# Performance work log

Hardware: AMD Instinct MI355X
Metric: run time of the kernel (lower is better)

Reference implementation:

```python
import jax, jax.numpy as jnp
import numpy as np

H = 512   # hidden_size
IN = 5    # input_size
OUT = 2   # output_size
B = 2048
T_HIST = 50


def _lstm_cell(x, h, c, W_ih, W_hh, b_ih, b_hh):
    # PyTorch gate order: i, f, g, o
    z = x @ W_ih.T + h @ W_hh.T + (b_ih + b_hh)
    i, f, g, o = jnp.split(z, 4, axis=-1)
    i = jax.nn.sigmoid(i)
    f = jax.nn.sigmoid(f)
    g = jnp.tanh(g)
    o = jax.nn.sigmoid(o)
    c2 = f * c + i * g
    h2 = o * jnp.tanh(c2)
    return h2, c2


def setup_inputs() -> dict:
    key = jax.random.key(0)
    ks = jax.random.split(key, 20)
    s = 0.05
    inp = {
        "history": jax.random.normal(ks[0], (B, T_HIST, IN), dtype=jnp.float32),
        "future_frames": 30,
        # encoder layer 0 (input IN) and layer 1 (input H)
        "enc_W_ih0": jax.random.normal(ks[1], (4 * H, IN)) * s,
        "enc_W_hh0": jax.random.normal(ks[2], (4 * H, H)) * s,
        "enc_b_ih0": jnp.zeros((4 * H,), jnp.float32),
        "enc_b_hh0": jnp.zeros((4 * H,), jnp.float32),
        "enc_W_ih1": jax.random.normal(ks[3], (4 * H, H)) * s,
        "enc_W_hh1": jax.random.normal(ks[4], (4 * H, H)) * s,
        "enc_b_ih1": jnp.zeros((4 * H,), jnp.float32),
        "enc_b_hh1": jnp.zeros((4 * H,), jnp.float32),
        # decoder layer 0 (input OUT) and layer 1 (input H)
        "dec_W_ih0": jax.random.normal(ks[5], (4 * H, OUT)) * s,
        "dec_W_hh0": jax.random.normal(ks[6], (4 * H, H)) * s,
        "dec_b_ih0": jnp.zeros((4 * H,), jnp.float32),
        "dec_b_hh0": jnp.zeros((4 * H,), jnp.float32),
        "dec_W_ih1": jax.random.normal(ks[7], (4 * H, H)) * s,
        "dec_W_hh1": jax.random.normal(ks[8], (4 * H, H)) * s,
        "dec_b_ih1": jnp.zeros((4 * H,), jnp.float32),
        "dec_b_hh1": jnp.zeros((4 * H,), jnp.float32),
        # output head
        "out_W": jax.random.normal(ks[9], (OUT, H)) * s,
        "out_b": jnp.zeros((OUT,), jnp.float32),
    }
    return inp


def reference(history, enc_W_ih0, enc_W_hh0, enc_b_ih0, enc_b_hh0,
              enc_W_ih1, enc_W_hh1, enc_b_ih1, enc_b_hh1,
              dec_W_ih0, dec_W_hh0, dec_b_ih0, dec_b_hh0,
              dec_W_ih1, dec_W_hh1, dec_b_ih1, dec_b_hh1,
              out_W, out_b, future_frames):
    batch = history.shape[0]
    z = jnp.zeros((batch, H), history.dtype)

    # ----- encoder: 2-layer LSTM over history, scan over time -----
    def enc_step(carry, x_t):
        h0, c0, h1, c1 = carry
        h0, c0 = _lstm_cell(x_t, h0, c0, enc_W_ih0, enc_W_hh0, enc_b_ih0, enc_b_hh0)
        h1, c1 = _lstm_cell(h0, h1, c1, enc_W_ih1, enc_W_hh1, enc_b_ih1, enc_b_hh1)
        return (h0, c0, h1, c1), None

    xs = jnp.swapaxes(history, 0, 1)  # [T, B, IN]
    (h0, c0, h1, c1), _ = jax.lax.scan(enc_step, (z, z, z, z), xs)

    def dec_step(carry, _):
        h0, c0, h1, c1, x_prev = carry
        h0, c0 = _lstm_cell(x_prev, h0, c0, dec_W_ih0, dec_W_hh0, dec_b_ih0, dec_b_hh0)
        h1, c1 = _lstm_cell(h0, h1, c1, dec_W_ih1, dec_W_hh1, dec_b_ih1, dec_b_hh1)
        pred = h1 @ out_W.T + out_b  # [B, OUT]
        return (h0, c0, h1, c1, pred), pred

    x0 = jnp.zeros((batch, OUT), history.dtype)
    _, preds = jax.lax.scan(dec_step, (h0, c0, h1, c1, x0), None, length=future_frames)
    return jnp.swapaxes(preds, 0, 1)  # [B, T_fut, OUT]
```

## Files before the change

kernel.cpp:

```cpp
#include <hip/hip_runtime.h>
#include <hip/hip_bf16.h>


#define HDIM 512
#define BDIM 2048
#define T_HIST 50
#define T_FUT 30

typedef __attribute__((ext_vector_type(8))) short short8;
typedef __attribute__((ext_vector_type(4))) float f32x4;

#define AS1(p) ((const __attribute__((address_space(1))) void*)(p))
#define AS3(p) ((__attribute__((address_space(3))) void*)(p))

__device__ __forceinline__ ushort f2bf(float f) {
    union { float f; unsigned u; } v; v.f = f;
    unsigned r = v.u + 0x7fff + ((v.u >> 16) & 1);
    return (ushort)(r >> 16);
}
__device__ __forceinline__ float bf2f(ushort h) {
    union { unsigned u; float f; } v; v.u = ((unsigned)h) << 16;
    return v.f;
}

__device__ __forceinline__ int swz(int row, int slot) {
    int q = row >> 1;
    int t = ((row & 1) << 2) | slot;
    return q * 8 + (t ^ (q & 7));
}

struct SplitSrc { const float* src[6]; };

__global__ __launch_bounds__(256) void split_weights(SplitSrc s, ushort* __restrict__ hi,
                                                     ushort* __restrict__ lo) {
    int row = blockIdx.x;
    int j = blockIdx.y;
    int g = row >> 9, u = row & 511;
    int rp = (u >> 5) * 128 + ((u >> 4) & 1) * 64 + g * 16 + (u & 15);
    const float* S = s.src[j] + (size_t)row * HDIM;
    ushort* H = hi + ((size_t)j * 2048 + rp) * HDIM;
    ushort* L = lo + ((size_t)j * 2048 + rp) * HDIM;
    for (int k = threadIdx.x; k < HDIM; k += 256) {
        float w = S[k];
        ushort hb = f2bf(w);
        H[k] = hb;
        L[k] = f2bf(w - bf2f(hb));
    }
}

struct CellDesc {
    const ushort *A1h, *A1l, *W1h, *W1l;
    const ushort *A2h, *A2l, *W2h, *W2l;
    const float *x; const float *Wx;
    const float *bih, *bhh;
    float* c; ushort *hh; ushort *hl;
    int np, xs, Kx;
};

__global__ __launch_bounds__(256, 2) void lstm_cells(CellDesc dA, CellDesc dB) {
    __shared__ __align__(16) ushort lds[2 * 16384];

    const CellDesc d = (blockIdx.x >> 8) ? dB : dA;

    const int tid = threadIdx.x;
    const int w = tid >> 6, l = tid & 63;
    const int wm = w >> 1, wn = w & 1;
    const int lrow = l & 15, lk = l >> 4;

    int id = blockIdx.x & 255;
    int xcd = id & 7, rr = id >> 3;
    int bx = (xcd & 3) * 4 + (rr & 3);
    int by = (xcd >> 2) * 8 + (rr >> 2);
    const int m0 = by * 128;
    const int n0 = bx * 128;
    const int u  = bx * 32 + wn * 16 + lrow;

    f32x4 acc[4][4];

    #pragma unroll
    for (int g = 0; g < 4; ++g) {
        float b = d.bih[g * HDIM + u] + d.bhh[g * HDIM + u];
        f32x4 bv = {b, b, b, b};
        #pragma unroll
        for (int fm = 0; fm < 4; ++fm) acc[fm][g] = bv;
    }
    if (d.Kx > 0) {
        for (int kx = 0; kx < d.Kx; ++kx) {
            float wv[4];
            #pragma unroll
            for (int g = 0; g < 4; ++g) wv[g] = d.Wx[(size_t)(g * HDIM + u) * d.Kx + kx];
            #pragma unroll
            for (int fm = 0; fm < 4; ++fm)
                #pragma unroll
                for (int r = 0; r < 4; ++r) {
                    int m = m0 + wm * 64 + fm * 16 + lk * 4 + r;
                    float xv = d.x[(size_t)m * d.xs + kx];
                    #pragma unroll
                    for (int g = 0; g < 4; ++g) acc[fm][g][r] += xv * wv[g];
                }
        }
    }

    auto STAGE = [&](int t) {
        int buf = t & 1;
        int p = t >> 4;
        int kc = (t & 15) * 32;
        const ushort* Ah = p ? d.A2h : d.A1h;
        const ushort* Al = p ? d.A2l : d.A1l;
        const ushort* Bh = p ? d.W2h : d.W1h;
        const ushort* Bl = p ? d.W2l : d.W1l;
        ushort* base = &lds[buf * 16384];
        #pragma unroll
        for (int it = 0; it < 2; ++it) {
            int db = (w * 2 + it) * 64;
            int dd = db + l;
            int q = dd >> 3, tp = dd & 7;
            int tl = tp ^ (q & 7);
            int r = (q << 1) | (tl >> 2);
            int s = tl & 3;
            size_t go = (size_t)r * HDIM + kc + s * 8;
            __builtin_amdgcn_global_load_lds(AS1(Ah + (size_t)m0 * HDIM + go),
                                             AS3(base + db * 8), 16, 0, 0);
            __builtin_amdgcn_global_load_lds(AS1(Al + (size_t)m0 * HDIM + go),
                                             AS3(base + 4096 + db * 8), 16, 0, 0);
            __builtin_amdgcn_global_load_lds(AS1(Bh + (size_t)n0 * HDIM + go),
                                             AS3(base + 8192 + db * 8), 16, 0, 0);
            __builtin_amdgcn_global_load_lds(AS1(Bl + (size_t)n0 * HDIM + go),
                                             AS3(base + 12288 + db * 8), 16, 0, 0);
        }
    };

    const int nch = d.np * 16;
    STAGE(0);

    for (int t = 0; t < nch; ++t) {
        __syncthreads();
        if (t + 1 < nch) STAGE(t + 1);
        ushort* base = &lds[(t & 1) * 16384];
        short8 ah[4], al[4], bh[4], bl[4];
        #pragma unroll
        for (int fm = 0; fm < 4; ++fm) {
            int row = wm * 64 + fm * 16 + lrow;
            int off = swz(row, lk) * 8;
            ah[fm] = *(const short8*)(base + off);
            al[fm] = *(const short8*)(base + 4096 + off);
        }
        #pragma unroll
        for (int g = 0; g < 4; ++g) {
            int row = wn * 64 + g * 16 + lrow;
            int off = swz(row, lk) * 8;
            bh[g] = *(const short8*)(base + 8192 + off);
            bl[g] = *(const short8*)(base + 12288 + off);
        }
        #pragma unroll
        for (int fm = 0; fm < 4; ++fm)
            #pragma unroll
            for (int g = 0; g < 4; ++g)
                acc[fm][g] = __builtin_amdgcn_mfma_f32_16x16x32_bf16(
                    ah[fm], bh[g], acc[fm][g], 0, 0, 0);
        #pragma unroll
        for (int fm = 0; fm < 4; ++fm)
            #pragma unroll
            for (int g = 0; g < 4; ++g)
                acc[fm][g] = __builtin_amdgcn_mfma_f32_16x16x32_bf16(
                    al[fm], bh[g], acc[fm][g], 0, 0, 0);
        #pragma unroll
        for (int fm = 0; fm < 4; ++fm)
            #pragma unroll
            for (int g = 0; g < 4; ++g)
                acc[fm][g] = __builtin_amdgcn_mfma_f32_16x16x32_bf16(
                    ah[fm], bl[g], acc[fm][g], 0, 0, 0);
    }

    #pragma unroll
    for (int fm = 0; fm < 4; ++fm)
        #pragma unroll
        for (int r = 0; r < 4; ++r) {
            int m = m0 + wm * 64 + fm * 16 + lk * 4 + r;
            size_t idx = (size_t)m * HDIM + u;
            float zi = acc[fm][0][r], zf = acc[fm][1][r];
            float zg = acc[fm][2][r], zo = acc[fm][3][r];
            float ig = 1.f / (1.f + __expf(-zi));
            float fg = 1.f / (1.f + __expf(-zf));
            float gg = 2.f / (1.f + __expf(-2.f * zg)) - 1.f;
            float og = 1.f / (1.f + __expf(-zo));
            float cn = fg * d.c[idx] + ig * gg;
            float hn = og * (2.f / (1.f + __expf(-2.f * cn)) - 1.f);
            d.c[idx] = cn;
            ushort hb = f2bf(hn);
            d.hh[idx] = hb;
            d.hl[idx] = f2bf(hn - bf2f(hb));
        }
}

__global__ __launch_bounds__(256) void head_kernel(
    const ushort* __restrict__ hhi, const ushort* __restrict__ hlo,
    const float* __restrict__ Wout, const float* __restrict__ bout,
    float* __restrict__ out, float* __restrict__ xbuf, int t)
{
    int wave = (blockIdx.x * 256 + threadIdx.x) >> 6;
    int lane = threadIdx.x & 63;
    const ushort* hr = hhi + (size_t)wave * HDIM;
    const ushort* lr = hlo + (size_t)wave * HDIM;
    float s0 = 0.f, s1 = 0.f;
    #pragma unroll
    for (int k = lane; k < HDIM; k += 64) {
        float hv = bf2f(hr[k]) + bf2f(lr[k]);
        s0 += hv * Wout[k];
        s1 += hv * Wout[HDIM + k];
    }
    #pragma unroll
    for (int off = 32; off > 0; off >>= 1) {
        s0 += __shfl_down(s0, off);
        s1 += __shfl_down(s1, off);
    }
    if (lane == 0) {
        float p0 = s0 + bout[0], p1 = s1 + bout[1];
        out[(size_t)wave * (T_FUT * 2) + t * 2 + 0] = p0;
        out[(size_t)wave * (T_FUT * 2) + t * 2 + 1] = p1;
        xbuf[wave * 2 + 0] = p0;
        xbuf[wave * 2 + 1] = p1;
    }
}

extern "C" void kernel_launch(void* const* d_in, const int* in_sizes, int n_in,
                              void* d_out, int out_size, void* d_ws, size_t ws_size,
                              hipStream_t stream) {
    const float* history = (const float*)d_in[0];
    const float* eWih0 = (const float*)d_in[2];
    const float* eWhh0 = (const float*)d_in[3];
    const float* ebih0 = (const float*)d_in[4];
    const float* ebhh0 = (const float*)d_in[5];
    const float* eWih1 = (const float*)d_in[6];
    const float* eWhh1 = (const float*)d_in[7];
    const float* ebih1 = (const float*)d_in[8];
    const float* ebhh1 = (const float*)d_in[9];
    const float* dWih0 = (const float*)d_in[10];
    const float* dWhh0 = (const float*)d_in[11];
    const float* dbih0 = (const float*)d_in[12];
    const float* dbhh0 = (const float*)d_in[13];
    const float* dWih1 = (const float*)d_in[14];
    const float* dWhh1 = (const float*)d_in[15];
    const float* dbih1 = (const float*)d_in[16];
    const float* dbhh1 = (const float*)d_in[17];
    const float* outW  = (const float*)d_in[18];
    const float* outb  = (const float*)d_in[19];
    float* out = (float*)d_out;

    const size_t M = (size_t)2048 * 512;
    ushort* whi = (ushort*)d_ws;
    ushort* wlo = whi + 6 * M;
    ushort* hb  = wlo + 6 * M;
    float*  c0  = (float*)(hb + 8 * M);
    float*  c1  = c0 + M;
    float*  xbuf = c1 + M;

    ushort* h0a_hi = hb + 0 * M; ushort* h0a_lo = hb + 1 * M;
    ushort* h0b_hi = hb + 2 * M; ushort* h0b_lo = hb + 3 * M;
    ushort* h1a_hi = hb + 4 * M; ushort* h1a_lo = hb + 5 * M;
    ushort* h1b_hi = hb + 6 * M; ushort* h1b_lo = hb + 7 * M;

    hipMemsetAsync(h0a_hi, 0, 2 * M * sizeof(ushort), stream);
    hipMemsetAsync(h1a_hi, 0, 2 * M * sizeof(ushort), stream);
    hipMemsetAsync(c0, 0, 2 * M * sizeof(float), stream);
    hipMemsetAsync(xbuf, 0, BDIM * 2 * sizeof(float), stream);

    SplitSrc ss;
    ss.src[0] = eWhh0; ss.src[1] = eWih1; ss.src[2] = eWhh1;
    ss.src[3] = dWhh0; ss.src[4] = dWih1; ss.src[5] = dWhh1;
    split_weights<<<dim3(2048, 6), 256, 0, stream>>>(ss, whi, wlo);

    #define WHI(j) (whi + (size_t)(j) * M)
    #define WLO(j) (wlo + (size_t)(j) * M)

    auto H0R_HI = [&](int s){ return (s & 1) ? h0b_hi : h0a_hi; };
    auto H0R_LO = [&](int s){ return (s & 1) ? h0b_lo : h0a_lo; };
    auto H0W_HI = [&](int s){ return (s & 1) ? h0a_hi : h0b_hi; };
    auto H0W_LO = [&](int s){ return (s & 1) ? h0a_lo : h0b_lo; };
    auto H1R_HI = [&](int s){ return (s & 1) ? h1b_hi : h1a_hi; };
    auto H1R_LO = [&](int s){ return (s & 1) ? h1b_lo : h1a_lo; };
    auto H1W_HI = [&](int s){ return (s & 1) ? h1a_hi : h1b_hi; };
    auto H1W_LO = [&](int s){ return (s & 1) ? h1a_lo : h1b_lo; };

    auto mkL0enc = [&](int s) {
        CellDesc d{};
        d.A1h = H0R_HI(s); d.A1l = H0R_LO(s); d.W1h = WHI(0); d.W1l = WLO(0);
        d.np = 1; d.x = history + s * 5; d.xs = T_HIST * 5; d.Kx = 5; d.Wx = eWih0;
        d.bih = ebih0; d.bhh = ebhh0; d.c = c0; d.hh = H0W_HI(s); d.hl = H0W_LO(s);
        return d;
    };
    auto mkL1enc = [&](int s) {
        CellDesc d{};
        d.A1h = H0W_HI(s); d.A1l = H0W_LO(s); d.W1h = WHI(1); d.W1l = WLO(1);
        d.A2h = H1R_HI(s); d.A2l = H1R_LO(s); d.W2h = WHI(2); d.W2l = WLO(2);
        d.np = 2; d.Kx = 0; d.xs = 0;
        d.bih = ebih1; d.bhh = ebhh1; d.c = c1; d.hh = H1W_HI(s); d.hl = H1W_LO(s);
        return d;
    };
    auto mkD0 = [&](int s) {
        CellDesc d{};
        d.A1h = H0R_HI(s); d.A1l = H0R_LO(s); d.W1h = WHI(3); d.W1l = WLO(3);
        d.np = 1; d.x = xbuf; d.xs = 2; d.Kx = 2; d.Wx = dWih0;
        d.bih = dbih0; d.bhh = dbhh0; d.c = c0; d.hh = H0W_HI(s); d.hl = H0W_LO(s);
        return d;
    };
    auto mkD1 = [&](int s) {
        CellDesc d{};
        d.A1h = H0W_HI(s); d.A1l = H0W_LO(s); d.W1h = WHI(4); d.W1l = WLO(4);
        d.A2h = H1R_HI(s); d.A2l = H1R_LO(s); d.W2h = WHI(5); d.W2l = WLO(5);
        d.np = 2; d.Kx = 0; d.xs = 0;
        d.bih = dbih1; d.bhh = dbhh1; d.c = c1; d.hh = H1W_HI(s); d.hl = H1W_LO(s);
        return d;
    };

    dim3 blk(256);

    {
        CellDesc d = mkL0enc(0);
        lstm_cells<<<256, blk, 0, stream>>>(d, d);
    }
    for (int s = 0; s < T_HIST; ++s) {
        CellDesc dL1 = mkL1enc(s);
        CellDesc dNx = (s + 1 < T_HIST) ? mkL0enc(s + 1) : mkD0(T_HIST);
        lstm_cells<<<512, blk, 0, stream>>>(dL1, dNx);
    }
    for (int s = T_HIST; s < T_HIST + T_FUT; ++s) {
        CellDesc d1 = mkD1(s);
        lstm_cells<<<256, blk, 0, stream>>>(d1, d1);
        head_kernel<<<512, blk, 0, stream>>>(H1W_HI(s), H1W_LO(s), outW, outb,
                                             out, xbuf, s - T_HIST);
        if (s + 1 < T_HIST + T_FUT) {
            CellDesc d0 = mkD0(s + 1);
            lstm_cells<<<256, blk, 0, stream>>>(d0, d0);
        }
    }
    #undef WHI
    #undef WLO
}
```

Measured before the change: 3.772 ms.

## Fuse output head into decoder layer-0 cell and load weights directly to registers

The per-step head kernel launch is removed. Each decoder layer-0 cell block now recomputes the previous step's projection for its 128 rows, keeps it in LDS as the fed-back input, and the bx==0 blocks write it to the output. Only the final step still uses the standalone head kernel. The GEMM loop also stops staging weight tiles through LDS: it loads them straight from global memory into registers, double-buffered, which halves the LDS footprint and the LDS traffic. The cost is that the head dot products are recomputed redundantly across the 16 column blocks, and the register-loaded weight fragments raise register pressure.

```diff
diff --git a/kernel.cpp b/kernel.cpp
--- a/kernel.cpp
+++ b/kernel.cpp
@@ -53,12 +53,15 @@
     const ushort *A2h, *A2l, *W2h, *W2l;
     const float *x; const float *Wx;
     const float *bih, *bhh;
+    const ushort *hsrc_hi, *hsrc_lo;
+    const float *Wout, *bout; float *out_t;
     float* c; ushort *hh; ushort *hl;
     int np, xs, Kx;
 };
 
 __global__ __launch_bounds__(256, 2) void lstm_cells(CellDesc dA, CellDesc dB) {
-    __shared__ __align__(16) ushort lds[2 * 16384];
+    __shared__ __align__(16) ushort lds[2 * 8192];
+    __shared__ float xlds[128][2];
 
     const CellDesc d = (blockIdx.x >> 8) ? dB : dA;
 
@@ -75,7 +78,87 @@
     const int n0 = bx * 128;
     const int u  = bx * 32 + wn * 16 + lrow;
 
+    size_t boff[4];
+    #pragma unroll
+    for (int g = 0; g < 4; ++g)
+        boff[g] = (size_t)(n0 + wn * 64 + g * 16 + lrow) * HDIM + lk * 8;
+
     f32x4 acc[4][4];
+
+#define STAGE(t)                                                              \
+    {                                                                         \
+        int p_ = (t) >> 4;                                                    \
+        int kc_ = ((t) & 15) * 32;                                            \
+        const ushort* Ah_ = p_ ? d.A2h : d.A1h;                               \
+        const ushort* Al_ = p_ ? d.A2l : d.A1l;                               \
+        ushort* sb_ = &lds[((t) & 1) * 8192];                                 \
+        _Pragma("unroll")                                                     \
+        for (int it = 0; it < 2; ++it) {                                      \
+            int db = (w * 2 + it) * 64;                                       \
+            int dd = db + l;                                                  \
+            int q_ = dd >> 3, tp_ = dd & 7;                                   \
+            int tl_ = tp_ ^ (q_ & 7);                                         \
+            int r_ = (q_ << 1) | (tl_ >> 2);                                  \
+            int s_ = tl_ & 3;                                                 \
+            size_t go_ = (size_t)(m0 + r_) * HDIM + kc_ + s_ * 8;             \
+            __builtin_amdgcn_global_load_lds(AS1(Ah_ + go_),                  \
+                                             AS3(sb_ + db * 8), 16, 0, 0);    \
+            __builtin_amdgcn_global_load_lds(AS1(Al_ + go_),                  \
+                                             AS3(sb_ + 4096 + db * 8), 16, 0, 0); \
+        }                                                                     \
+    }
+
+#define LOADB(t, bh_, bl_)                                                    \
+    {                                                                         \
+        int p_ = (t) >> 4;                                                    \
+        int kc_ = ((t) & 15) * 32;                                            \
+        const ushort* Bh_ = p_ ? d.W2h : d.W1h;                               \
+        const ushort* Bl_ = p_ ? d.W2l : d.W1l;                               \
+        _Pragma("unroll")                                                     \
+        for (int g = 0; g < 4; ++g) {                                         \
+            bh_[g] = *(const short8*)(Bh_ + boff[g] + kc_);                   \
+            bl_[g] = *(const short8*)(Bl_ + boff[g] + kc_);                   \
+        }                                                                     \
+    }
+
+#define ITER(t, bhc, blc, bhn, bln)                                           \
+    {                                                                         \
+        __syncthreads();                                                      \
+        if ((t) + 1 < nch) { STAGE((t) + 1); LOADB((t) + 1, bhn, bln); }      \
+        ushort* base = &lds[((t) & 1) * 8192];                                \
+        short8 ah[4], al[4];                                                  \
+        _Pragma("unroll")                                                     \
+        for (int fm = 0; fm < 4; ++fm) {                                      \
+            int row_ = wm * 64 + fm * 16 + lrow;                              \
+            int off_ = swz(row_, lk) * 8;                                     \
+            ah[fm] = *(const short8*)(base + off_);                           \
+            al[fm] = *(const short8*)(base + 4096 + off_);                    \
+        }                                                                     \
+        _Pragma("unroll")                                                     \
+        for (int fm = 0; fm < 4; ++fm)                                        \
+            _Pragma("unroll")                                                 \
+            for (int g = 0; g < 4; ++g)                                       \
+                acc[fm][g] = __builtin_amdgcn_mfma_f32_16x16x32_bf16(         \
+                    ah[fm], bhc[g], acc[fm][g], 0, 0, 0);                     \
+        _Pragma("unroll")                                                     \
+        for (int fm = 0; fm < 4; ++fm)                                        \
+            _Pragma("unroll")                                                 \
+            for (int g = 0; g < 4; ++g)                                       \
+                acc[fm][g] = __builtin_amdgcn_mfma_f32_16x16x32_bf16(         \
+                    al[fm], bhc[g], acc[fm][g], 0, 0, 0);                     \
+        _Pragma("unroll")                                                     \
+        for (int fm = 0; fm < 4; ++fm)                                        \
+            _Pragma("unroll")                                                 \
+            for (int g = 0; g < 4; ++g)                                       \
+                acc[fm][g] = __builtin_amdgcn_mfma_f32_16x16x32_bf16(         \
+                    ah[fm], blc[g], acc[fm][g], 0, 0, 0);                     \
+    }
+
+    const int nch = d.np * 16;
+
+    short8 bh0[4], bl0[4], bh1[4], bl1[4];
+    STAGE(0);
+    LOADB(0, bh0, bl0);
 
     #pragma unroll
     for (int g = 0; g < 4; ++g) {
@@ -84,6 +167,7 @@
         #pragma unroll
         for (int fm = 0; fm < 4; ++fm) acc[fm][g] = bv;
     }
+
     if (d.Kx > 0) {
         for (int kx = 0; kx < d.Kx; ++kx) {
             float wv[4];
@@ -101,75 +185,51 @@
         }
     }
 
-    auto STAGE = [&](int t) {
-        int buf = t & 1;
-        int p = t >> 4;
-        int kc = (t & 15) * 32;
-        const ushort* Ah = p ? d.A2h : d.A1h;
-        const ushort* Al = p ? d.A2l : d.A1l;
-        const ushort* Bh = p ? d.W2h : d.W1h;
-        const ushort* Bl = p ? d.W2l : d.W1l;
-        ushort* base = &lds[buf * 16384];
-        #pragma unroll
-        for (int it = 0; it < 2; ++it) {
-            int db = (w * 2 + it) * 64;
-            int dd = db + l;
-            int q = dd >> 3, tp = dd & 7;
-            int tl = tp ^ (q & 7);
-            int r = (q << 1) | (tl >> 2);
-            int s = tl & 3;
-            size_t go = (size_t)r * HDIM + kc + s * 8;
-            __builtin_amdgcn_global_load_lds(AS1(Ah + (size_t)m0 * HDIM + go),
-                                             AS3(base + db * 8), 16, 0, 0);
-            __builtin_amdgcn_global_load_lds(AS1(Al + (size_t)m0 * HDIM + go),
-                                             AS3(base + 4096 + db * 8), 16, 0, 0);
-            __builtin_amdgcn_global_load_lds(AS1(Bh + (size_t)n0 * HDIM + go),
-                                             AS3(base + 8192 + db * 8), 16, 0, 0);
-            __builtin_amdgcn_global_load_lds(AS1(Bl + (size_t)n0 * HDIM + go),
-                                             AS3(base + 12288 + db * 8), 16, 0, 0);
-        }
-    };
-
-    const int nch = d.np * 16;
-    STAGE(0);
-
-    for (int t = 0; t < nch; ++t) {
+    if (d.hsrc_hi) {
+        int row = tid >> 1, half = tid & 1;
+        const ushort* hh = d.hsrc_hi + (size_t)(m0 + row) * HDIM + half * 256;
+        const ushort* hl = d.hsrc_lo + (size_t)(m0 + row) * HDIM + half * 256;
+        float s0 = 0.f, s1 = 0.f;
+        #pragma unroll 4
+        for (int j = 0; j < 32; ++j) {
+            short8 a = *(const short8*)(hh + j * 8);
+            short8 b = *(const short8*)(hl + j * 8);
+            #pragma unroll
+            for (int e = 0; e < 8; ++e) {
+                float hv = bf2f((ushort)a[e]) + bf2f((ushort)b[e]);
+                int k = half * 256 + j * 8 + e;
+                s0 += hv * d.Wout[k];
+                s1 += hv * d.Wout[HDIM + k];
+            }
+        }
+        s0 += __shfl_xor(s0, 1);
+        s1 += __shfl_xor(s1, 1);
+        float x0 = s0 + d.bout[0], x1 = s1 + d.bout[1];
+        if (half == 0) {
+            xlds[row][0] = x0; xlds[row][1] = x1;
+            if (bx == 0 && d.out_t) {
+                d.out_t[(size_t)(m0 + row) * (T_FUT * 2) + 0] = x0;
+                d.out_t[(size_t)(m0 + row) * (T_FUT * 2) + 1] = x1;
+            }
+        }
         __syncthreads();
-        if (t + 1 < nch) STAGE(t + 1);
-        ushort* base = &lds[(t & 1) * 16384];
-        short8 ah[4], al[4], bh[4], bl[4];
-        #pragma unroll
-        for (int fm = 0; fm < 4; ++fm) {
-            int row = wm * 64 + fm * 16 + lrow;
-            int off = swz(row, lk) * 8;
-            ah[fm] = *(const short8*)(base + off);
-            al[fm] = *(const short8*)(base + 4096 + off);
-        }
         #pragma unroll
         for (int g = 0; g < 4; ++g) {
-            int row = wn * 64 + g * 16 + lrow;
-            int off = swz(row, lk) * 8;
-            bh[g] = *(const short8*)(base + 8192 + off);
-            bl[g] = *(const short8*)(base + 12288 + off);
-        }
-        #pragma unroll
-        for (int fm = 0; fm < 4; ++fm)
+            float w0 = d.Wx[(size_t)(g * HDIM + u) * 2 + 0];
+            float w1 = d.Wx[(size_t)(g * HDIM + u) * 2 + 1];
             #pragma unroll
-            for (int g = 0; g < 4; ++g)
-                acc[fm][g] = __builtin_amdgcn_mfma_f32_16x16x32_bf16(
-                    ah[fm], bh[g], acc[fm][g], 0, 0, 0);
-        #pragma unroll
-        for (int fm = 0; fm < 4; ++fm)
-            #pragma unroll
-            for (int g = 0; g < 4; ++g)
-                acc[fm][g] = __builtin_amdgcn_mfma_f32_16x16x32_bf16(
-                    al[fm], bh[g], acc[fm][g], 0, 0, 0);
-        #pragma unroll
-        for (int fm = 0; fm < 4; ++fm)
-            #pragma unroll
-            for (int g = 0; g < 4; ++g)
-                acc[fm][g] = __builtin_amdgcn_mfma_f32_16x16x32_bf16(
-                    ah[fm], bl[g], acc[fm][g], 0, 0, 0);
+            for (int fm = 0; fm < 4; ++fm)
+                #pragma unroll
+                for (int r = 0; r < 4; ++r) {
+                    int ml = wm * 64 + fm * 16 + lk * 4 + r;
+                    acc[fm][g][r] += xlds[ml][0] * w0 + xlds[ml][1] * w1;
+                }
+        }
+    }
+
+    for (int t = 0; t < nch; t += 2) {
+        ITER(t, bh0, bl0, bh1, bl1);
+        ITER(t + 1, bh1, bl1, bh0, bl0);
     }
 
     #pragma unroll
@@ -191,12 +251,15 @@
             d.hh[idx] = hb;
             d.hl[idx] = f2bf(hn - bf2f(hb));
         }
+#undef STAGE
+#undef LOADB
+#undef ITER
 }
 
 __global__ __launch_bounds__(256) void head_kernel(
     const ushort* __restrict__ hhi, const ushort* __restrict__ hlo,
     const float* __restrict__ Wout, const float* __restrict__ bout,
-    float* __restrict__ out, float* __restrict__ xbuf, int t)
+    float* __restrict__ out, int t)
 {
     int wave = (blockIdx.x * 256 + threadIdx.x) >> 6;
     int lane = threadIdx.x & 63;
@@ -215,11 +278,8 @@
         s1 += __shfl_down(s1, off);
     }
     if (lane == 0) {
-        float p0 = s0 + bout[0], p1 = s1 + bout[1];
-        out[(size_t)wave * (T_FUT * 2) + t * 2 + 0] = p0;
-        out[(size_t)wave * (T_FUT * 2) + t * 2 + 1] = p1;
-        xbuf[wave * 2 + 0] = p0;
-        xbuf[wave * 2 + 1] = p1;
+        out[(size_t)wave * (T_FUT * 2) + t * 2 + 0] = s0 + bout[0];
+        out[(size_t)wave * (T_FUT * 2) + t * 2 + 1] = s1 + bout[1];
     }
 }
 
@@ -253,7 +313,6 @@
     ushort* hb  = wlo + 6 * M;
     float*  c0  = (float*)(hb + 8 * M);
     float*  c1  = c0 + M;
-    float*  xbuf = c1 + M;
 
     ushort* h0a_hi = hb + 0 * M; ushort* h0a_lo = hb + 1 * M;
     ushort* h0b_hi = hb + 2 * M; ushort* h0b_lo = hb + 3 * M;
@@ -263,7 +322,6 @@
     hipMemsetAsync(h0a_hi, 0, 2 * M * sizeof(ushort), stream);
     hipMemsetAsync(h1a_hi, 0, 2 * M * sizeof(ushort), stream);
     hipMemsetAsync(c0, 0, 2 * M * sizeof(float), stream);
-    hipMemsetAsync(xbuf, 0, BDIM * 2 * sizeof(float), stream);
 
     SplitSrc ss;
     ss.src[0] = eWhh0; ss.src[1] = eWih1; ss.src[2] = eWhh1;
@@ -300,7 +358,12 @@
     auto mkD0 = [&](int s) {
         CellDesc d{};
         d.A1h = H0R_HI(s); d.A1l = H0R_LO(s); d.W1h = WHI(3); d.W1l = WLO(3);
-        d.np = 1; d.x = xbuf; d.xs = 2; d.Kx = 2; d.Wx = dWih0;
+        d.np = 1; d.Kx = 0; d.xs = 0; d.Wx = dWih0;
+        if (s > T_HIST) {
+            d.hsrc_hi = H1W_HI(s - 1); d.hsrc_lo = H1W_LO(s - 1);
+            d.Wout = outW; d.bout = outb;
+            d.out_t = out + (size_t)(s - T_HIST - 1) * 2;
+        }
         d.bih = dbih0; d.bhh = dbhh0; d.c = c0; d.hh = H0W_HI(s); d.hl = H0W_LO(s);
         return d;
     };
@@ -327,13 +390,14 @@
     for (int s = T_HIST; s < T_HIST + T_FUT; ++s) {
         CellDesc d1 = mkD1(s);
         lstm_cells<<<256, blk, 0, stream>>>(d1, d1);
-        head_kernel<<<512, blk, 0, stream>>>(H1W_HI(s), H1W_LO(s), outW, outb,
-                                             out, xbuf, s - T_HIST);
         if (s + 1 < T_HIST + T_FUT) {
             CellDesc d0 = mkD0(s + 1);
             lstm_cells<<<256, blk, 0, stream>>>(d0, d0);
         }
     }
+    head_kernel<<<512, blk, 0, stream>>>(
+        H1W_HI(T_HIST + T_FUT - 1), H1W_LO(T_HIST + T_FUT - 1),
+        outW, outb, out, T_FUT - 1);
     #undef WHI
     #undef WLO
 }
```

Result: slower. 6.714 ms (+78.0%).

## Fuse output head into next decoder layer-0 cell kernel, drop per-step head launch

Applied to the files above, without the earlier changes.

The linear output head (h1 to 2-dim prediction) is now computed inside the following decoder layer-0 lstm_cells launch. Each block recomputes predictions for its 128 rows into LDS and feeds them as the layer-0 input, and only blocks with bx==0 write them to the output. A separate head kernel runs only for the final step. This removes 29 kernel launches and the xbuf round trip. It also precomputes swizzled LDS offsets, moves bias/x init after the first stage prefetch, and raises wave priority around the MFMA section. The cost is that each column block redundantly recomputes the head dot products.

```diff
diff --git a/kernel.cpp b/kernel.cpp
--- a/kernel.cpp
+++ b/kernel.cpp
@@ -53,12 +53,15 @@
     const ushort *A2h, *A2l, *W2h, *W2l;
     const float *x; const float *Wx;
     const float *bih, *bhh;
+    const ushort *hsrc_hi, *hsrc_lo;
+    const float *Wout, *bout; float *out_t;
     float* c; ushort *hh; ushort *hl;
     int np, xs, Kx;
 };
 
 __global__ __launch_bounds__(256, 2) void lstm_cells(CellDesc dA, CellDesc dB) {
     __shared__ __align__(16) ushort lds[2 * 16384];
+    __shared__ float xlds[128][2];
 
     const CellDesc d = (blockIdx.x >> 8) ? dB : dA;
 
@@ -75,31 +78,15 @@
     const int n0 = bx * 128;
     const int u  = bx * 32 + wn * 16 + lrow;
 
+    int offA[4], offB[4];
+    #pragma unroll
+    for (int fm = 0; fm < 4; ++fm)
+        offA[fm] = swz(wm * 64 + fm * 16 + lrow, lk) * 8;
+    #pragma unroll
+    for (int g = 0; g < 4; ++g)
+        offB[g] = swz(wn * 64 + g * 16 + lrow, lk) * 8;
+
     f32x4 acc[4][4];
-
-    #pragma unroll
-    for (int g = 0; g < 4; ++g) {
-        float b = d.bih[g * HDIM + u] + d.bhh[g * HDIM + u];
-        f32x4 bv = {b, b, b, b};
-        #pragma unroll
-        for (int fm = 0; fm < 4; ++fm) acc[fm][g] = bv;
-    }
-    if (d.Kx > 0) {
-        for (int kx = 0; kx < d.Kx; ++kx) {
-            float wv[4];
-            #pragma unroll
-            for (int g = 0; g < 4; ++g) wv[g] = d.Wx[(size_t)(g * HDIM + u) * d.Kx + kx];
-            #pragma unroll
-            for (int fm = 0; fm < 4; ++fm)
-                #pragma unroll
-                for (int r = 0; r < 4; ++r) {
-                    int m = m0 + wm * 64 + fm * 16 + lk * 4 + r;
-                    float xv = d.x[(size_t)m * d.xs + kx];
-                    #pragma unroll
-                    for (int g = 0; g < 4; ++g) acc[fm][g][r] += xv * wv[g];
-                }
-        }
-    }
 
     auto STAGE = [&](int t) {
         int buf = t & 1;
@@ -133,6 +120,73 @@
     const int nch = d.np * 16;
     STAGE(0);
 
+    #pragma unroll
+    for (int g = 0; g < 4; ++g) {
+        float b = d.bih[g * HDIM + u] + d.bhh[g * HDIM + u];
+        f32x4 bv = {b, b, b, b};
+        #pragma unroll
+        for (int fm = 0; fm < 4; ++fm) acc[fm][g] = bv;
+    }
+
+    if (d.Kx > 0) {
+        for (int kx = 0; kx < d.Kx; ++kx) {
+            float wv[4];
+            #pragma unroll
+            for (int g = 0; g < 4; ++g) wv[g] = d.Wx[(size_t)(g * HDIM + u) * d.Kx + kx];
+            #pragma unroll
+            for (int fm = 0; fm < 4; ++fm)
+                #pragma unroll
+                for (int r = 0; r < 4; ++r) {
+                    int m = m0 + wm * 64 + fm * 16 + lk * 4 + r;
+                    float xv = d.x[(size_t)m * d.xs + kx];
+                    #pragma unroll
+                    for (int g = 0; g < 4; ++g) acc[fm][g][r] += xv * wv[g];
+                }
+        }
+    }
+
+    if (d.hsrc_hi) {
+        int row = tid >> 1, half = tid & 1;
+        const ushort* hh = d.hsrc_hi + (size_t)(m0 + row) * HDIM + half * 256;
+        const ushort* hl = d.hsrc_lo + (size_t)(m0 + row) * HDIM + half * 256;
+        float s0 = 0.f, s1 = 0.f;
+        #pragma unroll 4
+        for (int j = 0; j < 32; ++j) {
+            short8 a = *(const short8*)(hh + j * 8);
+            short8 b = *(const short8*)(hl + j * 8);
+            #pragma unroll
+            for (int e = 0; e < 8; ++e) {
+                float hv = bf2f((ushort)a[e]) + bf2f((ushort)b[e]);
+                int k = half * 256 + j * 8 + e;
+                s0 += hv * d.Wout[k];
+                s1 += hv * d.Wout[HDIM + k];
+            }
+        }
+        s0 += __shfl_xor(s0, 1);
+        s1 += __shfl_xor(s1, 1);
+        float x0 = s0 + d.bout[0], x1 = s1 + d.bout[1];
+        if (half == 0) {
+            xlds[row][0] = x0; xlds[row][1] = x1;
+            if (bx == 0 && d.out_t) {
+                d.out_t[(size_t)(m0 + row) * (T_FUT * 2) + 0] = x0;
+                d.out_t[(size_t)(m0 + row) * (T_FUT * 2) + 1] = x1;
+            }
+        }
+        __syncthreads();
+        #pragma unroll
+        for (int g = 0; g < 4; ++g) {
+            float w0 = d.Wx[(size_t)(g * HDIM + u) * 2 + 0];
+            float w1 = d.Wx[(size_t)(g * HDIM + u) * 2 + 1];
+            #pragma unroll
+            for (int fm = 0; fm < 4; ++fm)
+                #pragma unroll
+                for (int r = 0; r < 4; ++r) {
+                    int ml = wm * 64 + fm * 16 + lk * 4 + r;
+                    acc[fm][g][r] += xlds[ml][0] * w0 + xlds[ml][1] * w1;
+                }
+        }
+    }
+
     for (int t = 0; t < nch; ++t) {
         __syncthreads();
         if (t + 1 < nch) STAGE(t + 1);
@@ -140,18 +194,15 @@
         short8 ah[4], al[4], bh[4], bl[4];
         #pragma unroll
         for (int fm = 0; fm < 4; ++fm) {
-            int row = wm * 64 + fm * 16 + lrow;
-            int off = swz(row, lk) * 8;
-            ah[fm] = *(const short8*)(base + off);
-            al[fm] = *(const short8*)(base + 4096 + off);
+            ah[fm] = *(const short8*)(base + offA[fm]);
+            al[fm] = *(const short8*)(base + 4096 + offA[fm]);
         }
         #pragma unroll
         for (int g = 0; g < 4; ++g) {
-            int row = wn * 64 + g * 16 + lrow;
-            int off = swz(row, lk) * 8;
-            bh[g] = *(const short8*)(base + 8192 + off);
-            bl[g] = *(const short8*)(base + 12288 + off);
-        }
+            bh[g] = *(const short8*)(base + 8192 + offB[g]);
+            bl[g] = *(const short8*)(base + 12288 + offB[g]);
+        }
+        __builtin_amdgcn_s_setprio(1);
         #pragma unroll
         for (int fm = 0; fm < 4; ++fm)
             #pragma unroll
@@ -170,6 +221,7 @@
             for (int g = 0; g < 4; ++g)
                 acc[fm][g] = __builtin_amdgcn_mfma_f32_16x16x32_bf16(
                     ah[fm], bl[g], acc[fm][g], 0, 0, 0);
+        __builtin_amdgcn_s_setprio(0);
     }
 
     #pragma unroll
@@ -196,7 +248,7 @@
 __global__ __launch_bounds__(256) void head_kernel(
     const ushort* __restrict__ hhi, const ushort* __restrict__ hlo,
     const float* __restrict__ Wout, const float* __restrict__ bout,
-    float* __restrict__ out, float* __restrict__ xbuf, int t)
+    float* __restrict__ out, int t)
 {
     int wave = (blockIdx.x * 256 + threadIdx.x) >> 6;
     int lane = threadIdx.x & 63;
@@ -215,11 +267,8 @@
         s1 += __shfl_down(s1, off);
     }
     if (lane == 0) {
-        float p0 = s0 + bout[0], p1 = s1 + bout[1];
-        out[(size_t)wave * (T_FUT * 2) + t * 2 + 0] = p0;
-        out[(size_t)wave * (T_FUT * 2) + t * 2 + 1] = p1;
-        xbuf[wave * 2 + 0] = p0;
-        xbuf[wave * 2 + 1] = p1;
+        out[(size_t)wave * (T_FUT * 2) + t * 2 + 0] = s0 + bout[0];
+        out[(size_t)wave * (T_FUT * 2) + t * 2 + 1] = s1 + bout[1];
     }
 }
 
@@ -253,7 +302,6 @@
     ushort* hb  = wlo + 6 * M;
     float*  c0  = (float*)(hb + 8 * M);
     float*  c1  = c0 + M;
-    float*  xbuf = c1 + M;
 
     ushort* h0a_hi = hb + 0 * M; ushort* h0a_lo = hb + 1 * M;
     ushort* h0b_hi = hb + 2 * M; ushort* h0b_lo = hb + 3 * M;
@@ -263,7 +311,6 @@
     hipMemsetAsync(h0a_hi, 0, 2 * M * sizeof(ushort), stream);
     hipMemsetAsync(h1a_hi, 0, 2 * M * sizeof(ushort), stream);
     hipMemsetAsync(c0, 0, 2 * M * sizeof(float), stream);
-    hipMemsetAsync(xbuf, 0, BDIM * 2 * sizeof(float), stream);
 
     SplitSrc ss;
     ss.src[0] = eWhh0; ss.src[1] = eWih1; ss.src[2] = eWhh1;
@@ -300,7 +347,12 @@
     auto mkD0 = [&](int s) {
         CellDesc d{};
         d.A1h = H0R_HI(s); d.A1l = H0R_LO(s); d.W1h = WHI(3); d.W1l = WLO(3);
-        d.np = 1; d.x = xbuf; d.xs = 2; d.Kx = 2; d.Wx = dWih0;
+        d.np = 1; d.Kx = 0; d.xs = 0; d.Wx = dWih0;
+        if (s > T_HIST) {
+            d.hsrc_hi = H1W_HI(s - 1); d.hsrc_lo = H1W_LO(s - 1);
+            d.Wout = outW; d.bout = outb;
+            d.out_t = out + (size_t)(s - T_HIST - 1) * 2;
+        }
         d.bih = dbih0; d.bhh = dbhh0; d.c = c0; d.hh = H0W_HI(s); d.hl = H0W_LO(s);
         return d;
     };
@@ -327,13 +379,14 @@
     for (int s = T_HIST; s < T_HIST + T_FUT; ++s) {
         CellDesc d1 = mkD1(s);
         lstm_cells<<<256, blk, 0, stream>>>(d1, d1);
-        head_kernel<<<512, blk, 0, stream>>>(H1W_HI(s), H1W_LO(s), outW, outb,
-                                             out, xbuf, s - T_HIST);
         if (s + 1 < T_HIST + T_FUT) {
             CellDesc d0 = mkD0(s + 1);
             lstm_cells<<<256, blk, 0, stream>>>(d0, d0);
         }
     }
+    head_kernel<<<512, blk, 0, stream>>>(
+        H1W_HI(T_HIST + T_FUT - 1), H1W_LO(T_HIST + T_FUT - 1),
+        outW, outb, out, T_FUT - 1);
     #undef WHI
     #undef WLO
 }
```

Result: slower. 4.862 ms (+28.9%).

## Add larger-tile LSTM cell kernel for fused encoder steps

Applied to the files above, without the earlier changes.

Adds lstm_cells_big, which computes a 256x128 output tile per block (8x4 MFMA fragments per wave) with double-buffered LDS staging through global_load_lds, and an XCD-aware block-to-tile mapping. The encoder's combined layer-1/next-layer-0 launch moves from 512 blocks to 256 blocks of this kernel. Larger tiles raise arithmetic intensity and cut redundant weight and activation reloads. In exchange each block uses more registers and LDS, so occupancy drops to one block per CU and only 256 blocks are available to fill the GPU.

```diff
diff --git a/kernel.cpp b/kernel.cpp
--- a/kernel.cpp
+++ b/kernel.cpp
@@ -177,6 +177,146 @@
         #pragma unroll
         for (int r = 0; r < 4; ++r) {
             int m = m0 + wm * 64 + fm * 16 + lk * 4 + r;
+            size_t idx = (size_t)m * HDIM + u;
+            float zi = acc[fm][0][r], zf = acc[fm][1][r];
+            float zg = acc[fm][2][r], zo = acc[fm][3][r];
+            float ig = 1.f / (1.f + __expf(-zi));
+            float fg = 1.f / (1.f + __expf(-zf));
+            float gg = 2.f / (1.f + __expf(-2.f * zg)) - 1.f;
+            float og = 1.f / (1.f + __expf(-zo));
+            float cn = fg * d.c[idx] + ig * gg;
+            float hn = og * (2.f / (1.f + __expf(-2.f * cn)) - 1.f);
+            d.c[idx] = cn;
+            ushort hb = f2bf(hn);
+            d.hh[idx] = hb;
+            d.hl[idx] = f2bf(hn - bf2f(hb));
+        }
+}
+
+__global__ __launch_bounds__(256, 1) void lstm_cells_big(CellDesc dA, CellDesc dB) {
+    __shared__ __align__(16) ushort lds[2 * 24576];
+
+    const CellDesc d = (blockIdx.x >> 7) ? dB : dA;
+
+    const int tid = threadIdx.x;
+    const int w = tid >> 6, l = tid & 63;
+    const int wm = w >> 1, wn = w & 1;
+    const int lrow = l & 15, lk = l >> 4;
+
+    int id = blockIdx.x & 127;
+    int xcd = id & 7, rr = id >> 3;
+    int bx = (xcd & 3) * 4 + (rr & 3);
+    int by = (xcd >> 2) * 4 + (rr >> 2);
+    const int m0 = by * 256;
+    const int n0 = bx * 128;
+    const int u  = bx * 32 + wn * 16 + lrow;
+
+    f32x4 acc[8][4];
+
+    #pragma unroll
+    for (int g = 0; g < 4; ++g) {
+        float b = d.bih[g * HDIM + u] + d.bhh[g * HDIM + u];
+        f32x4 bv = {b, b, b, b};
+        #pragma unroll
+        for (int fm = 0; fm < 8; ++fm) acc[fm][g] = bv;
+    }
+    if (d.Kx > 0) {
+        for (int kx = 0; kx < d.Kx; ++kx) {
+            float wv[4];
+            #pragma unroll
+            for (int g = 0; g < 4; ++g) wv[g] = d.Wx[(size_t)(g * HDIM + u) * d.Kx + kx];
+            #pragma unroll
+            for (int fm = 0; fm < 8; ++fm)
+                #pragma unroll
+                for (int r = 0; r < 4; ++r) {
+                    int m = m0 + wm * 128 + fm * 16 + lk * 4 + r;
+                    float xv = d.x[(size_t)m * d.xs + kx];
+                    #pragma unroll
+                    for (int g = 0; g < 4; ++g) acc[fm][g][r] += xv * wv[g];
+                }
+        }
+    }
+
+    auto STAGE = [&](int t) {
+        int buf = t & 1;
+        int p = t >> 4;
+        int kc = (t & 15) * 32;
+        const ushort* Ah = p ? d.A2h : d.A1h;
+        const ushort* Al = p ? d.A2l : d.A1l;
+        const ushort* Bh = p ? d.W2h : d.W1h;
+        const ushort* Bl = p ? d.W2l : d.W1l;
+        ushort* base = &lds[buf * 24576];
+        #pragma unroll
+        for (int it = 0; it < 4; ++it) {
+            int db = (w * 4 + it) * 64;
+            int dd = db + l;
+            int q = dd >> 3, tp = dd & 7;
+            int tl = tp ^ (q & 7);
+            int r = (q << 1) | (tl >> 2);
+            int s = tl & 3;
+            size_t go = (size_t)r * HDIM + kc + s * 8;
+            __builtin_amdgcn_global_load_lds(AS1(Ah + (size_t)m0 * HDIM + go),
+                                             AS3(base + db * 8), 16, 0, 0);
+            __builtin_amdgcn_global_load_lds(AS1(Al + (size_t)m0 * HDIM + go),
+                                             AS3(base + 8192 + db * 8), 16, 0, 0);
+        }
+        #pragma unroll
+        for (int it = 0; it < 2; ++it) {
+            int db = (w * 2 + it) * 64;
+            int dd = db + l;
+            int q = dd >> 3, tp = dd & 7;
+            int tl = tp ^ (q & 7);
+            int r = (q << 1) | (tl >> 2);
+            int s = tl & 3;
+            size_t go = (size_t)r * HDIM + kc + s * 8;
+            __builtin_amdgcn_global_load_lds(AS1(Bh + (size_t)n0 * HDIM + go),
+                                             AS3(base + 16384 + db * 8), 16, 0, 0);
+            __builtin_amdgcn_global_load_lds(AS1(Bl + (size_t)n0 * HDIM + go),
+                                             AS3(base + 20480 + db * 8), 16, 0, 0);
+        }
+    };
+
+    const int nch = d.np * 16;
+    STAGE(0);
+
+    for (int t = 0; t < nch; ++t) {
+        __syncthreads();
+        if (t + 1 < nch) STAGE(t + 1);
+        ushort* base = &lds[(t & 1) * 24576];
+        short8 bh[4], bl[4];
+        #pragma unroll
+        for (int g = 0; g < 4; ++g) {
+            int row = wn * 64 + g * 16 + lrow;
+            int off = swz(row, lk) * 8;
+            bh[g] = *(const short8*)(base + 16384 + off);
+            bl[g] = *(const short8*)(base + 20480 + off);
+        }
+        #pragma unroll
+        for (int fm = 0; fm < 8; ++fm) {
+            int row = wm * 128 + fm * 16 + lrow;
+            int off = swz(row, lk) * 8;
+            short8 ah = *(const short8*)(base + off);
+            short8 al = *(const short8*)(base + 8192 + off);
+            #pragma unroll
+            for (int g = 0; g < 4; ++g)
+                acc[fm][g] = __builtin_amdgcn_mfma_f32_16x16x32_bf16(
+                    ah, bh[g], acc[fm][g], 0, 0, 0);
+            #pragma unroll
+            for (int g = 0; g < 4; ++g)
+                acc[fm][g] = __builtin_amdgcn_mfma_f32_16x16x32_bf16(
+                    al, bh[g], acc[fm][g], 0, 0, 0);
+            #pragma unroll
+            for (int g = 0; g < 4; ++g)
+                acc[fm][g] = __builtin_amdgcn_mfma_f32_16x16x32_bf16(
+                    ah, bl[g], acc[fm][g], 0, 0, 0);
+        }
+    }
+
+    #pragma unroll
+    for (int fm = 0; fm < 8; ++fm)
+        #pragma unroll
+        for (int r = 0; r < 4; ++r) {
+            int m = m0 + wm * 128 + fm * 16 + lk * 4 + r;
             size_t idx = (size_t)m * HDIM + u;
             float zi = acc[fm][0][r], zf = acc[fm][1][r];
             float zg = acc[fm][2][r], zo = acc[fm][3][r];
@@ -322,7 +462,7 @@
     for (int s = 0; s < T_HIST; ++s) {
         CellDesc dL1 = mkL1enc(s);
         CellDesc dNx = (s + 1 < T_HIST) ? mkL0enc(s + 1) : mkD0(T_HIST);
-        lstm_cells<<<512, blk, 0, stream>>>(dL1, dNx);
+        lstm_cells_big<<<256, blk, 0, stream>>>(dL1, dNx);
     }
     for (int s = T_HIST; s < T_HIST + T_FUT; ++s) {
         CellDesc d1 = mkD1(s);
```

Measured after the change: 4.274 ms. +13.3%, slower.
